# Performance work log

Hardware: AMD Instinct MI355X
Metric: run time of the kernel (lower is better)

## Reference

```python
import jax, jax.numpy as jnp
import numpy as np

L = 2        # num_layers
H = 512      # hidden_size
IN = 32      # input_size = output_size + 24
OUT = 8      # output_size
B = 512      # batch
S = 128      # encoder seq_len
F = 48       # future_len
TF = 24      # time-feature dim


def setup_inputs() -> dict:
    key = jax.random.key(0)
    ks = jax.random.split(key, 14)
    def rn(k, shape, s=0.05):
        return jax.random.normal(k, shape, dtype=jnp.float32) * s
    return {
        "x": rn(ks[0], (S, B, IN), 1.0),
        "future_time": rn(ks[1], (F - 1, B, TF), 1.0),
        "h0": rn(ks[2], (L, 1, H), 1.0),
        "c0": rn(ks[3], (L, 1, H), 1.0),
        # PyTorch nn.LSTM weights: gate order (i, f, g, o), rows of 4H
        "w_ih0": rn(ks[4], (4 * H, IN)),
        "w_hh0": rn(ks[5], (4 * H, H)),
        "b_ih0": rn(ks[6], (4 * H,)),
        "b_hh0": rn(ks[7], (4 * H,)),
        "w_ih1": rn(ks[8], (4 * H, H)),
        "w_hh1": rn(ks[9], (4 * H, H)),
        "b_ih1": rn(ks[10], (4 * H,)),
        "b_hh1": rn(ks[11], (4 * H,)),
        "fc_w": rn(ks[12], (OUT, H)),
        "fc_b": rn(ks[13], (OUT,)),
    }


def _cell(x, h, c, w_ih, w_hh, b):
    # PyTorch LSTMCell math, gate order i,f,g,o
    gates = x @ w_ih.T + h @ w_hh.T + b  # [B, 4H]
    i, f, g, o = jnp.split(gates, 4, axis=-1)
    c2 = jax.nn.sigmoid(f) * c + jax.nn.sigmoid(i) * jnp.tanh(g)
    h2 = jax.nn.sigmoid(o) * jnp.tanh(c2)
    return h2, c2


def reference(x, future_time, h0, c0,
              w_ih0, w_hh0, b_ih0, b_hh0,
              w_ih1, w_hh1, b_ih1, b_hh1,
              fc_w, fc_b):
    batch = x.shape[1]
    params = [(w_ih0, w_hh0, b_ih0 + b_hh0),
              (w_ih1, w_hh1, b_ih1 + b_hh1)]
    h_init = jnp.broadcast_to(h0, (L, batch, H))
    c_init = jnp.broadcast_to(c0, (L, batch, H))

    def multi_step(carry, x_t):
        hs, cs = carry
        new_h, new_c = [], []
        inp = x_t
        for l, (wi, wh, b) in enumerate(params):
            h2, c2 = _cell(inp, hs[l], cs[l], wi, wh, b)
            new_h.append(h2)
            new_c.append(c2)
            inp = h2
        return (jnp.stack(new_h), jnp.stack(new_c)), inp

    # encoder pass over the conditioning sequence
    (hs, cs), outs = jax.lax.scan(multi_step, (h_init, c_init), x)
    y0 = outs[-1] @ fc_w.T + fc_b  # [B, OUT], first prediction

    def dec_step(carry, t_feat):
        hs, cs, y = carry
        x_t = jnp.concatenate([y, t_feat], axis=-1)  # [B, OUT+TF] == [B, IN]
        (hs2, cs2), h_top = multi_step((hs, cs), x_t)
        y2 = h_top @ fc_w.T + fc_b
        return (hs2, cs2, y2), y2

    _, ys = jax.lax.scan(dec_step, (hs, cs, y0), future_time)
    return jnp.concatenate([y0[None], ys], axis=0)  # [future_len, B, OUT]
```

## Files before the change

kernel.cpp:

```cpp
#include <hip/hip_runtime.h>


typedef __attribute__((ext_vector_type(8))) short bf16x8;
typedef __attribute__((ext_vector_type(16))) float f32x16;

#define MFMA32(a, b, c) __builtin_amdgcn_mfma_f32_32x32x16_bf16((a), (b), (c), 0, 0, 0)
#define DEV static __device__ __forceinline__

constexpr int kSeq = 128;
constexpr int kT = 175;
constexpr int kRB = 65536;

constexpr size_t kWsHbuf = 0;
constexpr size_t kWsYacc = 2ull * 2 * 8 * kRB;
constexpr size_t kWsFlag = kWsYacc + 2ull * 512 * 8 * 4;
constexpr size_t kWsRc   = kWsFlag + 2ull * 8 * 32 * 64;
constexpr size_t kWsRd   = kWsRc + 2ull * 8 * 64;
constexpr size_t kWsEnd  = kWsRd + 8ull * 32 * 64;
constexpr size_t kWsZeroBegin = kWsYacc;
constexpr size_t kWsZeroSize  = kWsEnd - kWsYacc;

DEV unsigned short f2bf(float f) {
  unsigned u = __float_as_uint(f);
  u += 0x7fffu + ((u >> 16) & 1u);
  return (unsigned short)(u >> 16);
}
DEV float bf2f(unsigned short s) { return __uint_as_float(((unsigned)s) << 16); }
DEV float sigf(float v) { return 1.0f / (1.0f + __expf(-v)); }
DEV float tanhf_(float v) { float e = __expf(2.0f * v); return 1.0f - 2.0f / (e + 1.0f); }
DEV f32x16 zero16() {
  f32x16 z;
#pragma unroll
  for (int i = 0; i < 16; ++i) z[i] = 0.0f;
  return z;
}
DEV bf16x8 pack8(const float* p) {
  float4 a = *(const float4*)p;
  float4 b = *(const float4*)(p + 4);
  bf16x8 r;
  r[0] = (short)f2bf(a.x); r[1] = (short)f2bf(a.y);
  r[2] = (short)f2bf(a.z); r[3] = (short)f2bf(a.w);
  r[4] = (short)f2bf(b.x); r[5] = (short)f2bf(b.y);
  r[6] = (short)f2bf(b.z); r[7] = (short)f2bf(b.w);
  return r;
}

DEV unsigned ald(const unsigned* p) {
  return __hip_atomic_load(p, __ATOMIC_RELAXED, __HIP_MEMORY_SCOPE_AGENT);
}
DEV void ast(unsigned* p, unsigned v) {
  __hip_atomic_store(p, v, __ATOMIC_RELAXED, __HIP_MEMORY_SCOPE_AGENT);
}
DEV unsigned long long ald64(const unsigned long long* p) {
  return __hip_atomic_load(p, __ATOMIC_RELAXED, __HIP_MEMORY_SCOPE_AGENT);
}
DEV void ast64(unsigned long long* p, unsigned long long v) {
  __hip_atomic_store(p, v, __ATOMIC_RELAXED, __HIP_MEMORY_SCOPE_AGENT);
}
DEV float aldf(const float* p) {
  return __hip_atomic_load(p, __ATOMIC_RELAXED, __HIP_MEMORY_SCOPE_AGENT);
}
DEV void astf(float* p, float v) {
  __hip_atomic_store(p, v, __ATOMIC_RELAXED, __HIP_MEMORY_SCOPE_AGENT);
}
DEV void relwait() {
  __atomic_signal_fence(__ATOMIC_SEQ_CST);
  __builtin_amdgcn_s_waitcnt(0);
  __atomic_signal_fence(__ATOMIC_SEQ_CST);
}
DEV bool pollw(const unsigned* slot, unsigned thr) {
  for (int it = 0; it < (1 << 22); ++it) {
    const unsigned v = ald(slot);
    if (__ballot(v < thr) == 0ull) {
      __atomic_signal_fence(__ATOMIC_ACQUIRE);
      return true;
    }
    __builtin_amdgcn_s_sleep(8);
  }
  return false;
}

#define PARTS_WRITE(accv, ms_, ns_)                                           \
  { const int gate_ = (ns_)*2 + gbit;                                         \
    _Pragma("unroll") for (int rg = 0; rg < 16; ++rg) {                       \
      const int r_ = (ms_)*32 + (rg & 3) + 4 * hi5 + 8 * (rg >> 2);           \
      partsB[((kw * 4 + gate_) * 64 + r_) * 17 + l15] = f2bf((accv)[rg]);     \
    } }

__global__ __launch_bounds__(256, 2) void lstm_persist(
    const float* __restrict__ x, const float* __restrict__ ft,
    const float* __restrict__ h0in, const float* __restrict__ c0in,
    const float* __restrict__ wih0, const float* __restrict__ whh0,
    const float* __restrict__ bih0, const float* __restrict__ bhh0,
    const float* __restrict__ wih1, const float* __restrict__ whh1,
    const float* __restrict__ bih1, const float* __restrict__ bhh1,
    const float* __restrict__ fcw, const float* __restrict__ fcb,
    float* __restrict__ out, char* __restrict__ ws) {
  __shared__ __attribute__((aligned(16))) unsigned short partsB[16 * 64 * 17];
  __shared__ __attribute__((aligned(16))) unsigned short xin[64 * 40];
  __shared__ __attribute__((aligned(16))) unsigned short hloc[64 * 24];
  __shared__ float biasl[4][16];
  __shared__ float fcwl[8][16];
  __shared__ unsigned bflag;

  const int bid = blockIdx.x;
  const int layer = bid >> 8;
  const int idx = bid & 255;
  const int bc = idx & 7;
  const int hc = idx >> 3;
  const int b0 = bc * 64;
  const int u0 = hc * 16;
  const int tid = threadIdx.x;
  const int kw = tid >> 6;
  const int lane = tid & 63;
  const int l31 = lane & 31, l15 = lane & 15, hi5 = lane >> 5, gbit = (lane >> 4) & 1;

  char* hbuf = ws + kWsHbuf;
  float* yacc = (float*)(ws + kWsYacc);
  unsigned* flg = (unsigned*)(ws + kWsFlag);
  unsigned* rc = (unsigned*)(ws + kWsRc);
  unsigned* rdf = (unsigned*)(ws + kWsRd);

  auto fslot = [&](int l, int b, int h) { return flg + (((l * 8) + b) * 32 + h) * 16; };
  auto rdslot = [&](int b, int h) { return rdf + (b * 32 + h) * 16; };
  auto region = [&](int p, int l, int b) -> char* {
    return hbuf + (size_t)(((p * 2) + l) * 8 + b) * kRB;
  };

  bool alive = true;

  bf16x8 wf[2][16];
#pragma unroll
  for (int ns = 0; ns < 2; ++ns) {
    const int gate = ns * 2 + gbit;
    const int wrow = gate * 512 + u0 + l15;
    if (layer) {
#pragma unroll
      for (int m = 0; m < 16; ++m) {
        const int jg = kw + 4 * m;
        const int k0 = jg * 16 + hi5 * 8;
        const float* p = (k0 < 512) ? (wih1 + wrow * 512 + k0)
                                    : (whh1 + wrow * 512 + (k0 - 512));
        wf[ns][m] = pack8(p);
      }
    } else {
#pragma unroll
      for (int m = 0; m < 8; ++m) {
        const int jg = kw + 4 * m;
        wf[ns][m] = pack8(whh0 + wrow * 512 + jg * 16 + hi5 * 8);
      }
      if (kw < 2) wf[ns][8] = pack8(wih0 + wrow * 32 + kw * 16 + hi5 * 8);
    }
  }

  if (tid < 64) {
    const int g = tid >> 4, h = tid & 15;
    const int row = g * 512 + u0 + h;
    biasl[g][h] = layer ? (bih1[row] + bhh1[row]) : (bih0[row] + bhh0[row]);
  }
  if (layer && tid >= 64 && tid < 192) {
    const int t2 = tid - 64;
    fcwl[t2 >> 4][t2 & 15] = fcw[(t2 >> 4) * 512 + u0 + (t2 & 15)];
  }

  const int own_h = tid & 15;
  const int own_r0 = (tid >> 4) * 4;
  float cst[4];
  {
    const float cv = c0in[layer * 512 + u0 + own_h];
    cst[0] = cst[1] = cst[2] = cst[3] = cv;
  }

  {
    char* dst = region(layer ? 0 : 1, layer, bc);
    if (tid < 128) {
      const int r = tid >> 1, half = tid & 1;
      union { unsigned short s[8]; unsigned long long u[2]; } v;
#pragma unroll
      for (int k2 = 0; k2 < 8; ++k2)
        v.s[k2] = f2bf(h0in[layer * 512 + u0 + half * 8 + k2]);
      unsigned long long* dp =
          (unsigned long long*)(dst + ((u0 >> 3) + half) * 1024 + r * 16);
      ast64(dp, v.u[0]); ast64(dp + 1, v.u[1]);
    }
    relwait();
    __syncthreads();
    if (tid == 0) ast(fslot(layer, bc, hc), 1u);
  }

  auto xin_store = [&](int r, int c4, float4 v) {
    const int gx = c4 >> 3, half = (c4 >> 2) & 1;
    uint2 pv;
    pv.x = (unsigned)f2bf(v.x) | ((unsigned)f2bf(v.y) << 16);
    pv.y = (unsigned)f2bf(v.z) | ((unsigned)f2bf(v.w) << 16);
    *(uint2*)&xin[r * 40 + ((gx ^ (r & 3)) << 3) + half * 4] = pv;
  };

  auto cell_update = [&]() {
#pragma unroll
    for (int i = 0; i < 4; ++i) {
      const int r = own_r0 + i;
      float ig = biasl[0][own_h], fg = biasl[1][own_h];
      float gg = biasl[2][own_h], og = biasl[3][own_h];
#pragma unroll
      for (int w2 = 0; w2 < 4; ++w2) {
        ig += bf2f(partsB[((w2 * 4 + 0) * 64 + r) * 17 + own_h]);
        fg += bf2f(partsB[((w2 * 4 + 1) * 64 + r) * 17 + own_h]);
        gg += bf2f(partsB[((w2 * 4 + 2) * 64 + r) * 17 + own_h]);
        og += bf2f(partsB[((w2 * 4 + 3) * 64 + r) * 17 + own_h]);
      }
      const float cv = sigf(fg) * cst[i] + sigf(ig) * tanhf_(gg);
      cst[i] = cv;
      hloc[r * 24 + own_h] = f2bf(sigf(og) * tanhf_(cv));
    }
  };

  auto h_publish = [&](char* dst) {
    if (tid < 128) {
      const int r = tid >> 1, half = tid & 1;
      union { uint4 q; unsigned long long u[2]; } v;
      v.q = *(const uint4*)&hloc[r * 24 + half * 8];
      unsigned long long* dp =
          (unsigned long long*)(dst + ((u0 >> 3) + half) * 1024 + r * 16);
      ast64(dp, v.u[0]); ast64(dp + 1, v.u[1]);
    }
  };

  if (layer == 0) {
    for (int t = 0; t < kT; ++t) {
      if (kw == 0 && alive) {
        const unsigned* slot = (lane < 32)
            ? fslot(0, bc, lane)
            : ((t < kSeq) ? rdslot(bc, lane - 32) : fslot(1, bc, lane - 32));
        const unsigned thr = (lane < 32)
            ? (unsigned)(t + 1)
            : (unsigned)((t < kSeq) ? t : t + 1);
        alive = pollw(slot, thr);
      }
      __syncthreads();

      if (t < kSeq) {
#pragma unroll
        for (int it = 0; it < 2; ++it) {
          const int u = tid + it * 256;
          const int r = u >> 3, c4 = (u & 7) * 4;
          xin_store(r, c4, *(const float4*)&x[(size_t)(t * 512 + b0 + r) * 32 + c4]);
        }
        __syncthreads();
      } else {
        const int q = (t - 1) & 1;
        if (tid < 128) {
          const int r = tid >> 1, o4 = (tid & 1) * 4;
          const float* yp = &yacc[(size_t)(q * 512 + b0 + r) * 8 + o4];
          float4 v;
          v.x = aldf(yp + 0); v.y = aldf(yp + 1);
          v.z = aldf(yp + 2); v.w = aldf(yp + 3);
          const float4 bb = *(const float4*)&fcb[o4];
          v.x += bb.x; v.y += bb.y; v.z += bb.z; v.w += bb.w;
          if (hc == 0)
            *(float4*)&out[(size_t)((t - kSeq) * 512 + b0 + r) * 8 + o4] = v;
          xin_store(r, o4, v);
        }
        for (int u = tid; u < 384; u += 256) {
          const int r = u / 6, m = u - r * 6;
          xin_store(r, 8 + m * 4,
                    *(const float4*)&ft[(size_t)((t - kSeq) * 512 + b0 + r) * 24 + m * 4]);
        }
        __syncthreads();
        if (tid == 0) {
          const unsigned old = __hip_atomic_fetch_add(rc + (q * 8 + bc) * 16, 1u,
                                                      __ATOMIC_RELAXED,
                                                      __HIP_MEMORY_SCOPE_AGENT);
          bflag = (old == 31u) ? 1u : 0u;
        }
        __syncthreads();
        if (bflag) {
          for (int u = tid; u < 512; u += 256)
            astf(&yacc[(size_t)q * 512 * 8 + (size_t)b0 * 8 + u], 0.0f);
          relwait();
          __syncthreads();
          if (tid == 0) ast(rc + (q * 8 + bc) * 16, 0u);
        }
      }

      f32x16 acc00 = zero16(), acc01 = zero16(), acc10 = zero16(), acc11 = zero16();
      const char* hb0 = region((t - 1) & 1, 0, bc);
      unsigned long long abuf[2][16];
#pragma unroll
      for (int i = 0; i < 4; ++i) {
        const size_t off = (size_t)((2 * (kw + 4 * i) + hi5) * 64 + l31) * 16;
        const unsigned long long* p = (const unsigned long long*)(hb0 + off);
        abuf[0][i * 4 + 0] = ald64(p);
        abuf[0][i * 4 + 1] = ald64(p + 1);
        const unsigned long long* q2 = (const unsigned long long*)(hb0 + off + 512);
        abuf[0][i * 4 + 2] = ald64(q2);
        abuf[0][i * 4 + 3] = ald64(q2 + 1);
      }
#pragma unroll
      for (int g = 0; g < 2; ++g) {
        if (g == 0) {
#pragma unroll
          for (int i = 0; i < 4; ++i) {
            const int m = 4 + i;
            const size_t off = (size_t)((2 * (kw + 4 * m) + hi5) * 64 + l31) * 16;
            const unsigned long long* p = (const unsigned long long*)(hb0 + off);
            abuf[1][i * 4 + 0] = ald64(p);
            abuf[1][i * 4 + 1] = ald64(p + 1);
            const unsigned long long* q2 = (const unsigned long long*)(hb0 + off + 512);
            abuf[1][i * 4 + 2] = ald64(q2);
            abuf[1][i * 4 + 3] = ald64(q2 + 1);
          }
        }
#pragma unroll
        for (int i = 0; i < 4; ++i) {
          const int m = g * 4 + i;
          union { unsigned long long u[2]; bf16x8 v; } a0, a1;
          a0.u[0] = abuf[g][i * 4 + 0]; a0.u[1] = abuf[g][i * 4 + 1];
          a1.u[0] = abuf[g][i * 4 + 2]; a1.u[1] = abuf[g][i * 4 + 3];
          acc00 = MFMA32(a0.v, wf[0][m], acc00);
          acc01 = MFMA32(a0.v, wf[1][m], acc01);
          acc10 = MFMA32(a1.v, wf[0][m], acc10);
          acc11 = MFMA32(a1.v, wf[1][m], acc11);
        }
      }
      if (kw < 2) {
#pragma unroll
        for (int ms = 0; ms < 2; ++ms) {
          const int r = ms * 32 + l31;
          const int gx = kw * 2 + hi5;
          const bf16x8 a = *(const bf16x8*)&xin[r * 40 + ((gx ^ (r & 3)) << 3)];
          if (ms == 0) {
            acc00 = MFMA32(a, wf[0][8], acc00);
            acc01 = MFMA32(a, wf[1][8], acc01);
          } else {
            acc10 = MFMA32(a, wf[0][8], acc10);
            acc11 = MFMA32(a, wf[1][8], acc11);
          }
        }
      }
      PARTS_WRITE(acc00, 0, 0); PARTS_WRITE(acc01, 0, 1);
      PARTS_WRITE(acc10, 1, 0); PARTS_WRITE(acc11, 1, 1);
      __syncthreads();
      cell_update();
      __syncthreads();
      h_publish(region(t & 1, 0, bc));
      relwait();
      __syncthreads();
      if (tid == 0) ast(fslot(0, bc, hc), (unsigned)(t + 2));
    }
    if (hc == 0) {
      if (kw == 0 && alive)
        alive = pollw(fslot(1, bc, lane & 31), (unsigned)(kT + 1));
      __syncthreads();
      for (int u = tid; u < 512; u += 256) {
        const int r = u >> 3, o = u & 7;
        out[(size_t)(47 * 512 + b0 + r) * 8 + o] =
            aldf(&yacc[(size_t)(b0 + r) * 8 + o]) + fcb[o];
      }
    }
  } else {
    for (int t = 0; t < kT; ++t) {
      if (kw == 0 && alive) {
        const unsigned* slot = (lane < 32)
            ? fslot(0, bc, lane)
            : fslot(1, bc, lane - 32);
        const unsigned thr = (lane < 32) ? (unsigned)(t + 2) : (unsigned)(t + 1);
        alive = pollw(slot, thr);
      }
      __syncthreads();

      f32x16 acc00 = zero16(), acc01 = zero16(), acc10 = zero16(), acc11 = zero16();
      const char* hbA = region(t & 1, 0, bc);
      const char* hbB = region(t & 1, 1, bc);
      unsigned long long abuf[2][16];
#pragma unroll
      for (int i = 0; i < 4; ++i) {
        const char* base = hbA;
        const size_t off = (size_t)((2 * (kw + 4 * i) + hi5) * 64 + l31) * 16;
        const unsigned long long* p = (const unsigned long long*)(base + off);
        abuf[0][i * 4 + 0] = ald64(p);
        abuf[0][i * 4 + 1] = ald64(p + 1);
        const unsigned long long* q2 = (const unsigned long long*)(base + off + 512);
        abuf[0][i * 4 + 2] = ald64(q2);
        abuf[0][i * 4 + 3] = ald64(q2 + 1);
      }
#pragma unroll
      for (int g = 0; g < 4; ++g) {
        if (g < 3) {
          const int gn = g + 1;
#pragma unroll
          for (int i = 0; i < 4; ++i) {
            const int m = gn * 4 + i;
            const char* base = (m < 8) ? hbA : hbB;
            const int jl = (kw + 4 * m) & 31;
            const size_t off = (size_t)((2 * jl + hi5) * 64 + l31) * 16;
            const unsigned long long* p = (const unsigned long long*)(base + off);
            abuf[gn & 1][i * 4 + 0] = ald64(p);
            abuf[gn & 1][i * 4 + 1] = ald64(p + 1);
            const unsigned long long* q2 = (const unsigned long long*)(base + off + 512);
            abuf[gn & 1][i * 4 + 2] = ald64(q2);
            abuf[gn & 1][i * 4 + 3] = ald64(q2 + 1);
          }
        }
#pragma unroll
        for (int i = 0; i < 4; ++i) {
          const int m = g * 4 + i;
          union { unsigned long long u[2]; bf16x8 v; } a0, a1;
          a0.u[0] = abuf[g & 1][i * 4 + 0]; a0.u[1] = abuf[g & 1][i * 4 + 1];
          a1.u[0] = abuf[g & 1][i * 4 + 2]; a1.u[1] = abuf[g & 1][i * 4 + 3];
          acc00 = MFMA32(a0.v, wf[0][m], acc00);
          acc01 = MFMA32(a0.v, wf[1][m], acc01);
          acc10 = MFMA32(a1.v, wf[0][m], acc10);
          acc11 = MFMA32(a1.v, wf[1][m], acc11);
        }
      }
      PARTS_WRITE(acc00, 0, 0); PARTS_WRITE(acc01, 0, 1);
      PARTS_WRITE(acc10, 1, 0); PARTS_WRITE(acc11, 1, 1);
      __syncthreads();
      if (tid == 0) ast(rdslot(bc, hc), (unsigned)(t + 2));
      cell_update();
      __syncthreads();
      h_publish(region((t & 1) ^ 1, 1, bc));
      if (t >= kSeq - 1) {
        const int q = t & 1;
#pragma unroll
        for (int rep = 0; rep < 2; ++rep) {
          const int i2 = tid + rep * 256;
          const int r = i2 >> 3, o = i2 & 7;
          float s = 0.0f;
#pragma unroll
          for (int h2 = 0; h2 < 16; ++h2)
            s += bf2f(hloc[r * 24 + h2]) * fcwl[o][h2];
          atomicAdd(&yacc[(size_t)(q * 512 + b0 + r) * 8 + o], s);
        }
      }
      relwait();
      __syncthreads();
      if (tid == 0) ast(fslot(1, bc, hc), (unsigned)(t + 2));
    }
  }
}

extern "C" void kernel_launch(void* const* d_in, const int* in_sizes, int n_in,
                              void* d_out, int out_size, void* d_ws, size_t ws_size,
                              hipStream_t stream) {
  (void)in_sizes; (void)n_in; (void)out_size; (void)ws_size;
  hipMemsetAsync((char*)d_ws + kWsZeroBegin, 0, kWsZeroSize, stream);

  const float* x    = (const float*)d_in[0];
  const float* ft   = (const float*)d_in[1];
  const float* h0in = (const float*)d_in[2];
  const float* c0in = (const float*)d_in[3];
  const float* wih0 = (const float*)d_in[4];
  const float* whh0 = (const float*)d_in[5];
  const float* bih0 = (const float*)d_in[6];
  const float* bhh0 = (const float*)d_in[7];
  const float* wih1 = (const float*)d_in[8];
  const float* whh1 = (const float*)d_in[9];
  const float* bih1 = (const float*)d_in[10];
  const float* bhh1 = (const float*)d_in[11];
  const float* fcw  = (const float*)d_in[12];
  const float* fcb  = (const float*)d_in[13];
  float* out = (float*)d_out;
  char* ws = (char*)d_ws;

  void* args[] = {&x, &ft, &h0in, &c0in, &wih0, &whh0, &bih0, &bhh0,
                  &wih1, &whh1, &bih1, &bhh1, &fcw, &fcb, &out, &ws};
  hipError_t err = hipLaunchCooperativeKernel((void*)lstm_persist, dim3(512),
                                              dim3(256), args, 0, stream);
  if (err != hipSuccess) {
    lstm_persist<<<dim3(512), dim3(256), 0, stream>>>(
        x, ft, h0in, c0in, wih0, whh0, bih0, bhh0,
        wih1, whh1, bih1, bhh1, fcw, fcb, out, ws);
  }
}
```

Measured before the change: 3.390 ms.

## Double-buffer layer-0 input staging and interleave layer blocks across the grid

```diff
diff --git a/kernel.cpp b/kernel.cpp
--- a/kernel.cpp
+++ b/kernel.cpp
@@ -97,15 +97,15 @@
     const float* __restrict__ fcw, const float* __restrict__ fcb,
     float* __restrict__ out, char* __restrict__ ws) {
   __shared__ __attribute__((aligned(16))) unsigned short partsB[16 * 64 * 17];
-  __shared__ __attribute__((aligned(16))) unsigned short xin[64 * 40];
+  __shared__ __attribute__((aligned(16))) unsigned short xin[2][64 * 40];
   __shared__ __attribute__((aligned(16))) unsigned short hloc[64 * 24];
   __shared__ float biasl[4][16];
   __shared__ float fcwl[8][16];
   __shared__ unsigned bflag;
 
   const int bid = blockIdx.x;
-  const int layer = bid >> 8;
-  const int idx = bid & 255;
+  const int layer = bid & 1;
+  const int idx = bid >> 1;
   const int bc = idx & 7;
   const int hc = idx >> 3;
   const int b0 = bc * 64;
@@ -171,6 +171,14 @@
     cst[0] = cst[1] = cst[2] = cst[3] = cv;
   }
 
+  auto xin_store = [&](unsigned short* xb, int r, int c4, float4 v) {
+    const int gx = c4 >> 3, half = (c4 >> 2) & 1;
+    uint2 pv;
+    pv.x = (unsigned)f2bf(v.x) | ((unsigned)f2bf(v.y) << 16);
+    pv.y = (unsigned)f2bf(v.z) | ((unsigned)f2bf(v.w) << 16);
+    *(uint2*)&xb[r * 40 + ((gx ^ (r & 3)) << 3) + half * 4] = pv;
+  };
+
   {
     char* dst = region(layer ? 0 : 1, layer, bc);
     if (tid < 128) {
@@ -183,18 +191,18 @@
           (unsigned long long*)(dst + ((u0 >> 3) + half) * 1024 + r * 16);
       ast64(dp, v.u[0]); ast64(dp + 1, v.u[1]);
     }
+    if (layer == 0) {
+#pragma unroll
+      for (int it = 0; it < 2; ++it) {
+        const int u = tid + it * 256;
+        const int r = u >> 3, c4 = (u & 7) * 4;
+        xin_store(xin[0], r, c4, *(const float4*)&x[(size_t)(b0 + r) * 32 + c4]);
+      }
+    }
     relwait();
     __syncthreads();
     if (tid == 0) ast(fslot(layer, bc, hc), 1u);
   }
-
-  auto xin_store = [&](int r, int c4, float4 v) {
-    const int gx = c4 >> 3, half = (c4 >> 2) & 1;
-    uint2 pv;
-    pv.x = (unsigned)f2bf(v.x) | ((unsigned)f2bf(v.y) << 16);
-    pv.y = (unsigned)f2bf(v.z) | ((unsigned)f2bf(v.w) << 16);
-    *(uint2*)&xin[r * 40 + ((gx ^ (r & 3)) << 3) + half * 4] = pv;
-  };
 
   auto cell_update = [&]() {
 #pragma unroll
@@ -228,6 +236,7 @@
 
   if (layer == 0) {
     for (int t = 0; t < kT; ++t) {
+      const int p = t & 1;
       if (kw == 0 && alive) {
         const unsigned* slot = (lane < 32)
             ? fslot(0, bc, lane)
@@ -240,13 +249,21 @@
       __syncthreads();
 
       if (t < kSeq) {
-#pragma unroll
-        for (int it = 0; it < 2; ++it) {
-          const int u = tid + it * 256;
-          const int r = u >> 3, c4 = (u & 7) * 4;
-          xin_store(r, c4, *(const float4*)&x[(size_t)(t * 512 + b0 + r) * 32 + c4]);
-        }
-        __syncthreads();
+        if (t + 1 < kSeq) {
+#pragma unroll
+          for (int it = 0; it < 2; ++it) {
+            const int u = tid + it * 256;
+            const int r = u >> 3, c4 = (u & 7) * 4;
+            xin_store(xin[p ^ 1], r, c4,
+                      *(const float4*)&x[(size_t)((t + 1) * 512 + b0 + r) * 32 + c4]);
+          }
+        } else {
+          for (int u = tid; u < 384; u += 256) {
+            const int r = u / 6, m = u - r * 6;
+            xin_store(xin[p ^ 1], r, 8 + m * 4,
+                      *(const float4*)&ft[(size_t)(b0 + r) * 24 + m * 4]);
+          }
+        }
       } else {
         const int q = (t - 1) & 1;
         if (tid < 128) {
@@ -259,12 +276,14 @@
           v.x += bb.x; v.y += bb.y; v.z += bb.z; v.w += bb.w;
           if (hc == 0)
             *(float4*)&out[(size_t)((t - kSeq) * 512 + b0 + r) * 8 + o4] = v;
-          xin_store(r, o4, v);
-        }
-        for (int u = tid; u < 384; u += 256) {
-          const int r = u / 6, m = u - r * 6;
-          xin_store(r, 8 + m * 4,
-                    *(const float4*)&ft[(size_t)((t - kSeq) * 512 + b0 + r) * 24 + m * 4]);
+          xin_store(xin[p], r, o4, v);
+        }
+        if (t + 1 < kT) {
+          for (int u = tid; u < 384; u += 256) {
+            const int r = u / 6, m = u - r * 6;
+            xin_store(xin[p ^ 1], r, 8 + m * 4,
+                      *(const float4*)&ft[(size_t)((t + 1 - kSeq) * 512 + b0 + r) * 24 + m * 4]);
+          }
         }
         __syncthreads();
         if (tid == 0) {
@@ -289,9 +308,9 @@
 #pragma unroll
       for (int i = 0; i < 4; ++i) {
         const size_t off = (size_t)((2 * (kw + 4 * i) + hi5) * 64 + l31) * 16;
-        const unsigned long long* p = (const unsigned long long*)(hb0 + off);
-        abuf[0][i * 4 + 0] = ald64(p);
-        abuf[0][i * 4 + 1] = ald64(p + 1);
+        const unsigned long long* p2 = (const unsigned long long*)(hb0 + off);
+        abuf[0][i * 4 + 0] = ald64(p2);
+        abuf[0][i * 4 + 1] = ald64(p2 + 1);
         const unsigned long long* q2 = (const unsigned long long*)(hb0 + off + 512);
         abuf[0][i * 4 + 2] = ald64(q2);
         abuf[0][i * 4 + 3] = ald64(q2 + 1);
@@ -303,9 +322,9 @@
           for (int i = 0; i < 4; ++i) {
             const int m = 4 + i;
             const size_t off = (size_t)((2 * (kw + 4 * m) + hi5) * 64 + l31) * 16;
-            const unsigned long long* p = (const unsigned long long*)(hb0 + off);
-            abuf[1][i * 4 + 0] = ald64(p);
-            abuf[1][i * 4 + 1] = ald64(p + 1);
+            const unsigned long long* p2 = (const unsigned long long*)(hb0 + off);
+            abuf[1][i * 4 + 0] = ald64(p2);
+            abuf[1][i * 4 + 1] = ald64(p2 + 1);
             const unsigned long long* q2 = (const unsigned long long*)(hb0 + off + 512);
             abuf[1][i * 4 + 2] = ald64(q2);
             abuf[1][i * 4 + 3] = ald64(q2 + 1);
@@ -328,7 +347,7 @@
         for (int ms = 0; ms < 2; ++ms) {
           const int r = ms * 32 + l31;
           const int gx = kw * 2 + hi5;
-          const bf16x8 a = *(const bf16x8*)&xin[r * 40 + ((gx ^ (r & 3)) << 3)];
+          const bf16x8 a = *(const bf16x8*)&xin[p][r * 40 + ((gx ^ (r & 3)) << 3)];
           if (ms == 0) {
             acc00 = MFMA32(a, wf[0][8], acc00);
             acc01 = MFMA32(a, wf[1][8], acc01);
@@ -377,9 +396,9 @@
       for (int i = 0; i < 4; ++i) {
         const char* base = hbA;
         const size_t off = (size_t)((2 * (kw + 4 * i) + hi5) * 64 + l31) * 16;
-        const unsigned long long* p = (const unsigned long long*)(base + off);
-        abuf[0][i * 4 + 0] = ald64(p);
-        abuf[0][i * 4 + 1] = ald64(p + 1);
+        const unsigned long long* p2 = (const unsigned long long*)(base + off);
+        abuf[0][i * 4 + 0] = ald64(p2);
+        abuf[0][i * 4 + 1] = ald64(p2 + 1);
         const unsigned long long* q2 = (const unsigned long long*)(base + off + 512);
         abuf[0][i * 4 + 2] = ald64(q2);
         abuf[0][i * 4 + 3] = ald64(q2 + 1);
@@ -394,9 +413,9 @@
             const char* base = (m < 8) ? hbA : hbB;
             const int jl = (kw + 4 * m) & 31;
             const size_t off = (size_t)((2 * jl + hi5) * 64 + l31) * 16;
-            const unsigned long long* p = (const unsigned long long*)(base + off);
-            abuf[gn & 1][i * 4 + 0] = ald64(p);
-            abuf[gn & 1][i * 4 + 1] = ald64(p + 1);
+            const unsigned long long* p2 = (const unsigned long long*)(base + off);
+            abuf[gn & 1][i * 4 + 0] = ald64(p2);
+            abuf[gn & 1][i * 4 + 1] = ald64(p2 + 1);
             const unsigned long long* q2 = (const unsigned long long*)(base + off + 512);
             abuf[gn & 1][i * 4 + 2] = ald64(q2);
             abuf[gn & 1][i * 4 + 3] = ald64(q2 + 1);
```

New measurement: 5.391 ms. 1.59x slower.
